# Kernel optimization log

Hardware: AMD Instinct MI355X
Metric: run time of the kernel (lower is better)

The kernel has to match this reference:

```python
import jax, jax.numpy as jnp
import numpy as np

D = 64      # in_features
U = 1024    # hidden units
B = 4096    # batch

def _build_masks():
    d0 = np.arange(D)
    dh = np.arange(U) % (D - 1)
    m0 = (d0[None, :] <= dh[:, None]).astype(np.float32)          # [U, D]
    m1 = (dh[None, :] <= dh[:, None]).astype(np.float32)          # [U, U]
    m2 = np.tile((dh[None, :] < d0[:, None]).astype(np.float32), (2, 1))  # [2D, U]
    return jnp.asarray(m0), jnp.asarray(m1), jnp.asarray(m2)


def setup_inputs() -> dict:
    key = jax.random.key(0)
    ks = jax.random.split(key, 7)
    scale = 0.02  # small init so exp(sigma) stays finite
    return {
        "u": jax.random.normal(ks[0], (B, D), dtype=jnp.float32),
        "W0": jax.random.normal(ks[1], (U, D), dtype=jnp.float32) * scale,
        "b0": jax.random.normal(ks[2], (U,), dtype=jnp.float32) * scale,
        "W1": jax.random.normal(ks[3], (U, U), dtype=jnp.float32) * scale,
        "b1": jax.random.normal(ks[4], (U,), dtype=jnp.float32) * scale,
        "W2": jax.random.normal(ks[5], (2 * D, U), dtype=jnp.float32) * scale,
        "b2": jax.random.normal(ks[6], (2 * D,), dtype=jnp.float32) * scale,
    }


def reference(u, W0, b0, W1, b1, W2, b2):
    m0, m1, m2 = _build_masks()
    mW0, mW1, mW2 = m0 * W0, m1 * W1, m2 * W2  # masked weights (constant across steps)

    def made(x):  # x: [B, D] -> mu, sigma each [B, D]
        h = jax.nn.relu(x @ mW0.T + b0)
        h = jax.nn.relu(h @ mW1.T + b1)
        z = h @ mW2.T + b2
        return z[:, :D], z[:, D:]

    def step(carry, i):
        x, ldj = carry
        mu, sigma = made(x)
        # ordering = arange(D) (sequential, not reversed) => idx == i
        x = x.at[:, i].set(u[:, i] * jnp.exp(sigma[:, i]) + mu[:, i])
        ldj = ldj.at[:, i].set(sigma[:, i])
        return (x, ldj), None

    x0 = jnp.zeros_like(u)
    ldj0 = jnp.zeros_like(u)
    (x, ldj), _ = jax.lax.scan(step, (x0, ldj0), jnp.arange(D))
    log_det_jacobian = jnp.sum(ldj, axis=1, keepdims=True)  # [B, 1]
    return x, log_det_jacobian
```

## Files before the change

### kernel.cpp

```cpp
#include <hip/hip_runtime.h>
#include <hip/hip_bf16.h>

#define BATCH 4096
#define NTHR 512

typedef __attribute__((ext_vector_type(8))) short bf16x8;
typedef __attribute__((ext_vector_type(4))) float f32x4;
typedef __attribute__((ext_vector_type(4))) short short4v;

#define BAR() asm volatile("s_waitcnt lgkmcnt(0)\n\ts_barrier" ::: "memory")

__host__ __device__ __forceinline__ int off1(int g) { return (g <= 16) ? 17 * g : 16 * g + 16; }
__host__ __device__ __forceinline__ int cntg(int g) { return (g < 16) ? 17 : 16; }
__host__ __device__ __forceinline__ int unitOf(int p) {
    int gp, jp;
    if (p < 272) { gp = p / 17; jp = p - gp * 17; }
    else         { gp = (p >> 4) - 1; jp = p & 15; }
    return gp + 63 * jp;
}
__device__ __forceinline__ short f2bf(float f) {
    __hip_bfloat16 h = __float2bfloat16(f);
    return *reinterpret_cast<short*>(&h);
}

__global__ void prep5(const float* __restrict__ W0, const float* __restrict__ b0,
                      const float* __restrict__ W1, const float* __restrict__ b1,
                      const float* __restrict__ W2,
                      short* __restrict__ W1f, short* __restrict__ W2f,
                      short* __restrict__ W0f, float* __restrict__ b1p) {
    __shared__ short ws[16][1024];
    const int b = blockIdx.x, t = threadIdx.x;
    if (b < 72) {
        const bool isW1 = (b < 64);
        const int n = t >> 4;
        int u;
        if (isW1) u = unitOf(b * 16 + n);
        else {
            const int c = b - 64;
            u = (n & 1) ? (64 + c * 8 + (n >> 1)) : (c * 8 + (n >> 1));
        }
        const float* src = isW1 ? (W1 + (long)u * 1024) : (W2 + (long)u * 1024);
        const int c0 = (t & 15) * 4;
#pragma unroll
        for (int j = 0; j < 16; ++j) {
            int c = c0 + j * 64;
            float4 v = *(const float4*)&src[c];
            short4v sv;
            sv[0] = f2bf(v.x); sv[1] = f2bf(v.y); sv[2] = f2bf(v.z); sv[3] = f2bf(v.w);
            *(short4v*)&ws[n][c] = sv;
        }
        __syncthreads();
#pragma unroll 1
        for (int it = 0; it < 16; ++it) {
            int v = t + it * 256;
            if (v < 4032) {
                int g = v >> 6, lane2 = v & 63;
                int nn = lane2 & 15, aq2 = lane2 >> 4;
                bf16x8 pk;
#pragma unroll
                for (int e = 0; e < 8; ++e) {
                    int k = aq2 * 8 + e;
                    pk[e] = (k < cntg(g)) ? ws[nn][g + 63 * k] : (short)0;
                }
                if (isW1) *(bf16x8*)&W1f[(((long)g * 64 + b) * 64 + lane2) * 8] = pk;
                else      *(bf16x8*)&W2f[(((long)g * 8 + (b - 64)) * 64 + lane2) * 8] = pk;
            }
        }
    } else if (b < 88) {
        const int bb = b - 72;
#pragma unroll 1
        for (int j = 0; j < 32; ++j) {
            int q = t + j * 256;
            if (q < 8064) {
                int idx = bb * 8064 + q;
                int g = idx >> 11, rem = idx & 2047;
                int n2 = rem >> 10, kt = (rem >> 9) & 1, lane2 = (rem >> 3) & 63, e = rem & 7;
                int sl = n2 * 16 + (lane2 & 15);
                int kp = kt * 32 + ((lane2 >> 4) << 3) + e;
                float val = 0.f;
                if (sl < cntg(g)) {
                    int u = unitOf(off1(g) + sl);
                    if (kp == 0) val = b0[u];
                    else if (kp - 1 <= g) val = W0[u * 64 + kp - 1];
                }
                W0f[idx] = f2bf(val);
            }
        }
    } else {
        for (int p = t; p < 1024; p += 256) b1p[p] = b1[unitOf(p)];
    }
}

__global__ __launch_bounds__(NTHR, 2) void made5(
    const float* __restrict__ uin, const float* __restrict__ b2,
    const short* __restrict__ W1f, const short* __restrict__ W2f,
    const short* __restrict__ W0f, const float* __restrict__ b1p,
    float* __restrict__ out) {

    __shared__ __align__(16) short h1g[16][40];
    __shared__ __align__(16) short h2g[16][40];
    __shared__ __align__(16) short xhist[16][80];
    __shared__ __align__(16) float uT[64][16];
    __shared__ __align__(16) float xLs[16][68];
    __shared__ float ldjpart[8][16];

    const int t = threadIdx.x, lane = t & 63, wv = t >> 6;
    const int n = lane & 15, aq = lane >> 4;
    const int rowbase = blockIdx.x * 16;

    {
        int* z1 = (int*)&h1g[0][0];
        for (int idx = t; idx < 16 * 40 / 2; idx += NTHR) z1[idx] = 0;
        int* z2 = (int*)&h2g[0][0];
        for (int idx = t; idx < 16 * 40 / 2; idx += NTHR) z2[idx] = 0;
        int* z3 = (int*)&xhist[0][0];
        for (int idx = t; idx < 16 * 80 / 2; idx += NTHR) z3[idx] = 0;
    }
    if (t < 256) {
        int r = t >> 4, c0 = (t & 15) * 4;
        float4 v = *(const float4*)&uin[(long)(rowbase + r) * 64 + c0];
        uT[c0 + 0][r] = v.x; uT[c0 + 1][r] = v.y; uT[c0 + 2][r] = v.z; uT[c0 + 3][r] = v.w;
    }

    f32x4 acc2[8];
#pragma unroll
    for (int s = 0; s < 8; ++s) {
        float bb = b1p[(wv * 8 + s) * 16 + n];
        acc2[s] = (f32x4){bb, bb, bb, bb};
    }
    f32x4 zacc;
    {
        int pc = wv * 16 + n;
        float bz = b2[(pc >> 1) + 64 * (pc & 1)];
        zacc = (f32x4){bz, bz, bz, bz};
    }

    bf16x8 w1fE[8], w1fO[8], w2fE, w2fO, w0f[4];
#pragma unroll
    for (int s = 0; s < 8; ++s) {
        w1fO[s] = *(const bf16x8*)&W1f[(((long)0 * 64 + (wv * 8 + s)) * 64 + lane) * 8];
        w1fE[s] = *(const bf16x8*)&W1f[(((long)1 * 64 + (wv * 8 + s)) * 64 + lane) * 8];
    }
    w2fO = *(const bf16x8*)&W2f[(((long)0 * 8 + wv) * 64 + lane) * 8];
    w2fE = *(const bf16x8*)&W2f[(((long)1 * 8 + wv) * 64 + lane) * 8];
    if (wv == 7) {
#pragma unroll
        for (int f = 0; f < 4; ++f)
            w0f[f] = *(const bf16x8*)&W0f[(((long)0 * 4 + f) * 64 + lane) * 8];
    }

    f32x4 ldjacc = {0.f, 0.f, 0.f, 0.f};
    float ureg[4];

    BAR();
    if (t < 16) xhist[t][0] = (short)0x3F80;
#pragma unroll
    for (int r = 0; r < 4; ++r)
        ureg[r] = uT[8 * wv + (n >> 1)][aq * 4 + r];

    auto body = [&](int i, bf16x8* w1fS, bf16x8& w2fS) {
        const int g = i - 1;

        if (g >= 0 && wv == 7) {
            const int cgg = cntg(g);
            const bool two_k = (g >= 31);
            const bf16x8 ax0 = *(const bf16x8*)&xhist[n][aq * 8];
            f32x4 d0 = {0.f, 0.f, 0.f, 0.f};
            d0 = __builtin_amdgcn_mfma_f32_16x16x32_bf16(ax0, w0f[0], d0, 0, 0, 0);
            f32x4 d1 = {0.f, 0.f, 0.f, 0.f};
            if (two_k) {
                const bf16x8 ax1 = *(const bf16x8*)&xhist[n][32 + aq * 8];
                d0 = __builtin_amdgcn_mfma_f32_16x16x32_bf16(ax1, w0f[1], d0, 0, 0, 0);
                if (cgg == 17) {
                    d1 = __builtin_amdgcn_mfma_f32_16x16x32_bf16(ax0, w0f[2], d1, 0, 0, 0);
                    d1 = __builtin_amdgcn_mfma_f32_16x16x32_bf16(ax1, w0f[3], d1, 0, 0, 0);
                }
            } else if (cgg == 17) {
                d1 = __builtin_amdgcn_mfma_f32_16x16x32_bf16(ax0, w0f[2], d1, 0, 0, 0);
            }
            {
                const int gW = (i < 63) ? i : 62;
#pragma unroll
                for (int f = 0; f < 4; ++f)
                    w0f[f] = *(const bf16x8*)&W0f[(((long)gW * 4 + f) * 64 + lane) * 8];
            }
#pragma unroll
            for (int r = 0; r < 4; ++r) {
                float v = d0[r];
                h1g[aq * 4 + r][n] = f2bf(v > 0.f ? v : 0.f);
            }
            if (n == 0) {
#pragma unroll
                for (int r = 0; r < 4; ++r) {
                    float v = (cgg == 17) ? (d1[r] > 0.f ? d1[r] : 0.f) : 0.f;
                    h1g[aq * 4 + r][16] = f2bf(v);
                }
            }
        }
        BAR();

        if (g >= 0) {
            const int og = off1(g), cg = cntg(g);
            const int tf0 = og >> 4, tfl = (og + cg - 1) >> 4;
            const bf16x8 af = *(const bf16x8*)&h1g[n][aq * 8];
            const int s0 = tf0 - wv * 8;
#pragma unroll
            for (int s = 0; s < 8; ++s) {
                if (s >= s0)
                    acc2[s] = __builtin_amdgcn_mfma_f32_16x16x32_bf16(af, w1fS[s], acc2[s], 0, 0, 0);
            }
            if (i >= 1) {
                const int gp = (i + 1 < 63) ? (i + 1) : 62;
                const int s0p = (off1(gp) >> 4) - wv * 8;
#pragma unroll
                for (int s = 0; s < 8; ++s) {
                    if (s >= s0p)
                        w1fS[s] = *(const bf16x8*)&W1f[(((long)gp * 64 + (wv * 8 + s)) * 64 + lane) * 8];
                }
            }
            if (wv == (tf0 >> 3)) {
                const int s = tf0 & 7;
                const int j = tf0 * 16 + n - og;
                if (j >= 0 && j < cg) {
#pragma unroll
                    for (int r = 0; r < 4; ++r) {
                        float v = acc2[s][r];
                        h2g[aq * 4 + r][j] = f2bf(v > 0.f ? v : 0.f);
                    }
                }
            }
            if (tfl != tf0 && wv == (tfl >> 3)) {
                const int s = tfl & 7;
                const int j = tfl * 16 + n - og;
                if (j < cg) {
#pragma unroll
                    for (int r = 0; r < 4; ++r) {
                        float v = acc2[s][r];
                        h2g[aq * 4 + r][j] = f2bf(v > 0.f ? v : 0.f);
                    }
                }
            }
            if (g == 16 && wv == 0 && n == 0) {
#pragma unroll
                for (int r = 0; r < 4; ++r) h2g[aq * 4 + r][16] = 0;
            }
        }
        BAR();

        if (g >= 0) {
            const bf16x8 af3 = *(const bf16x8*)&h2g[n][aq * 8];
            zacc = __builtin_amdgcn_mfma_f32_16x16x32_bf16(af3, w2fS, zacc, 0, 0, 0);
            if (i >= 1) {
                const int gp = (i + 1 < 63) ? (i + 1) : 62;
                w2fS = *(const bf16x8*)&W2f[(((long)gp * 8 + wv) * 64 + lane) * 8];
            }
        }
        if (wv == (i >> 3)) {
            const int n0 = 2 * (i & 7);
            f32x4 sgv;
#pragma unroll
            for (int r = 0; r < 4; ++r) sgv[r] = __shfl_xor(zacc[r], 1);
            if (n == n0) {
#pragma unroll
                for (int r = 0; r < 4; ++r) {
                    const float sg = sgv[r], mu = zacc[r];
                    const float x = ureg[r] * __expf(sg) + mu;
                    ldjacc[r] += sg;
                    const int m = aq * 4 + r;
                    xLs[m][i] = x;
                    if (i < 63) xhist[m][i + 1] = f2bf(x);
                }
            }
        }
        BAR();
    };

#pragma unroll 1
    for (int i = 0; i < 64; i += 2) {
        body(i, w1fE, w2fE);
        body(i + 1, w1fO, w2fO);
    }

#pragma unroll
    for (int r = 0; r < 4; ++r) {
        float v = ldjacc[r];
        v += __shfl_xor(v, 2);
        v += __shfl_xor(v, 4);
        v += __shfl_xor(v, 8);
        if (n == 0) ldjpart[wv][aq * 4 + r] = v;
    }
    BAR();

    if (t < 256) {
        int r = t >> 4, c = (t & 15) * 4;
        float4 v;
        v.x = xLs[r][c]; v.y = xLs[r][c + 1]; v.z = xLs[r][c + 2]; v.w = xLs[r][c + 3];
        *(float4*)&out[(long)(rowbase + r) * 64 + c] = v;
    }
    if (t < 16) {
        float s = 0.f;
#pragma unroll
        for (int w = 0; w < 8; ++w) s += ldjpart[w][t];
        out[(long)BATCH * 64 + rowbase + t] = s;
    }
}

extern "C" void kernel_launch(void* const* d_in, const int* in_sizes, int n_in,
                              void* d_out, int out_size, void* d_ws, size_t ws_size,
                              hipStream_t stream) {
    (void)in_sizes; (void)n_in; (void)out_size; (void)ws_size;
    const float* u  = (const float*)d_in[0];
    const float* W0 = (const float*)d_in[1];
    const float* b0 = (const float*)d_in[2];
    const float* W1 = (const float*)d_in[3];
    const float* b1 = (const float*)d_in[4];
    const float* W2 = (const float*)d_in[5];
    const float* b2 = (const float*)d_in[6];
    float* out = (float*)d_out;

    short* W1f = (short*)d_ws;
    short* W2f = (short*)((char*)d_ws + 4128768);
    short* W0f = (short*)((char*)d_ws + 4128768 + 516096);
    float* b1p = (float*)((char*)d_ws + 4128768 + 516096 + 258048);

    prep5<<<dim3(89), dim3(256), 0, stream>>>(W0, b0, W1, b1, W2, W1f, W2f, W0f, b1p);
    made5<<<dim3(BATCH / 16), dim3(NTHR), 0, stream>>>(u, b2, W1f, W2f, W0f, b1p, out);
}
```

Baseline: 209.5 us.

## Fuse layer-0 MFMA into x-update phase, interleave W1 tiles across waves

The layer-0 MFMA and its h1 write move out of their own barrier-separated phase and into the wave that just produced the new x column, which removes one barrier per step. W1 tile ownership changes from contiguous (wv*8+s) to strided (wv+8*s), so the growing active tile range is spread across all waves instead of landing on a few. The prep kernel is relaunched with 512 threads. The new schedule depends on wave wv==i>>3 seeing its own xhist write, and only one wave does the layer-0 work on the critical path.

```diff
diff --git a/kernel.cpp b/kernel.cpp
--- a/kernel.cpp
+++ b/kernel.cpp
@@ -23,7 +23,7 @@
     return *reinterpret_cast<short*>(&h);
 }
 
-__global__ void prep5(const float* __restrict__ W0, const float* __restrict__ b0,
+__global__ void prep6(const float* __restrict__ W0, const float* __restrict__ b0,
                       const float* __restrict__ W1, const float* __restrict__ b1,
                       const float* __restrict__ W2,
                       short* __restrict__ W1f, short* __restrict__ W2f,
@@ -32,18 +32,15 @@
     const int b = blockIdx.x, t = threadIdx.x;
     if (b < 72) {
         const bool isW1 = (b < 64);
-        const int n = t >> 4;
+        const int n = t >> 5;
         int u;
         if (isW1) u = unitOf(b * 16 + n);
-        else {
-            const int c = b - 64;
-            u = (n & 1) ? (64 + c * 8 + (n >> 1)) : (c * 8 + (n >> 1));
-        }
+        else { const int c = b - 64; u = (n & 1) ? (64 + c * 8 + (n >> 1)) : (c * 8 + (n >> 1)); }
         const float* src = isW1 ? (W1 + (long)u * 1024) : (W2 + (long)u * 1024);
-        const int c0 = (t & 15) * 4;
-#pragma unroll
-        for (int j = 0; j < 16; ++j) {
-            int c = c0 + j * 64;
+        const int c0 = (t & 31) * 4;
+#pragma unroll
+        for (int j = 0; j < 8; ++j) {
+            int c = c0 + j * 128;
             float4 v = *(const float4*)&src[c];
             short4v sv;
             sv[0] = f2bf(v.x); sv[1] = f2bf(v.y); sv[2] = f2bf(v.z); sv[3] = f2bf(v.w);
@@ -51,8 +48,8 @@
         }
         __syncthreads();
 #pragma unroll 1
-        for (int it = 0; it < 16; ++it) {
-            int v = t + it * 256;
+        for (int it = 0; it < 8; ++it) {
+            int v = t + it * 512;
             if (v < 4032) {
                 int g = v >> 6, lane2 = v & 63;
                 int nn = lane2 & 15, aq2 = lane2 >> 4;
@@ -69,8 +66,8 @@
     } else if (b < 88) {
         const int bb = b - 72;
 #pragma unroll 1
-        for (int j = 0; j < 32; ++j) {
-            int q = t + j * 256;
+        for (int j = 0; j < 16; ++j) {
+            int q = t + j * 512;
             if (q < 8064) {
                 int idx = bb * 8064 + q;
                 int g = idx >> 11, rem = idx & 2047;
@@ -87,11 +84,11 @@
             }
         }
     } else {
-        for (int p = t; p < 1024; p += 256) b1p[p] = b1[unitOf(p)];
-    }
-}
-
-__global__ __launch_bounds__(NTHR, 2) void made5(
+        for (int p = t; p < 1024; p += 512) b1p[p] = b1[unitOf(p)];
+    }
+}
+
+__global__ __launch_bounds__(NTHR, 2) void made6(
     const float* __restrict__ uin, const float* __restrict__ b2,
     const short* __restrict__ W1f, const short* __restrict__ W2f,
     const short* __restrict__ W0f, const float* __restrict__ b1p,
@@ -125,7 +122,7 @@
     f32x4 acc2[8];
 #pragma unroll
     for (int s = 0; s < 8; ++s) {
-        float bb = b1p[(wv * 8 + s) * 16 + n];
+        float bb = b1p[(wv + 8 * s) * 16 + n];
         acc2[s] = (f32x4){bb, bb, bb, bb};
     }
     f32x4 zacc;
@@ -135,107 +132,69 @@
         zacc = (f32x4){bz, bz, bz, bz};
     }
 
-    bf16x8 w1fE[8], w1fO[8], w2fE, w2fO, w0f[4];
+    bf16x8 w1fE[8], w1fO[8], w2fE, w2fO, w0f0, w0f1, w0f2;
 #pragma unroll
     for (int s = 0; s < 8; ++s) {
-        w1fO[s] = *(const bf16x8*)&W1f[(((long)0 * 64 + (wv * 8 + s)) * 64 + lane) * 8];
-        w1fE[s] = *(const bf16x8*)&W1f[(((long)1 * 64 + (wv * 8 + s)) * 64 + lane) * 8];
+        const int tile = wv + 8 * s;
+        w1fO[s] = *(const bf16x8*)&W1f[(((long)0 * 64 + tile) * 64 + lane) * 8];
+        w1fE[s] = *(const bf16x8*)&W1f[(((long)1 * 64 + tile) * 64 + lane) * 8];
     }
     w2fO = *(const bf16x8*)&W2f[(((long)0 * 8 + wv) * 64 + lane) * 8];
     w2fE = *(const bf16x8*)&W2f[(((long)1 * 8 + wv) * 64 + lane) * 8];
-    if (wv == 7) {
-#pragma unroll
-        for (int f = 0; f < 4; ++f)
-            w0f[f] = *(const bf16x8*)&W0f[(((long)0 * 4 + f) * 64 + lane) * 8];
+    {
+        const long gb = 8 * wv;
+        w0f0 = *(const bf16x8*)&W0f[((gb * 4 + 0) * 64 + lane) * 8];
+        w0f1 = *(const bf16x8*)&W0f[((gb * 4 + 1) * 64 + lane) * 8];
+        w0f2 = *(const bf16x8*)&W0f[((gb * 4 + 2) * 64 + lane) * 8];
     }
 
     f32x4 ldjacc = {0.f, 0.f, 0.f, 0.f};
-    float ureg[4];
-
     BAR();
     if (t < 16) xhist[t][0] = (short)0x3F80;
-#pragma unroll
-    for (int r = 0; r < 4; ++r)
-        ureg[r] = uT[8 * wv + (n >> 1)][aq * 4 + r];
+    float ureg[4];
+#pragma unroll
+    for (int r = 0; r < 4; ++r) ureg[r] = uT[8 * wv + (n >> 1)][aq * 4 + r];
 
     auto body = [&](int i, bf16x8* w1fS, bf16x8& w2fS) {
         const int g = i - 1;
-
-        if (g >= 0 && wv == 7) {
-            const int cgg = cntg(g);
-            const bool two_k = (g >= 31);
-            const bf16x8 ax0 = *(const bf16x8*)&xhist[n][aq * 8];
-            f32x4 d0 = {0.f, 0.f, 0.f, 0.f};
-            d0 = __builtin_amdgcn_mfma_f32_16x16x32_bf16(ax0, w0f[0], d0, 0, 0, 0);
-            f32x4 d1 = {0.f, 0.f, 0.f, 0.f};
-            if (two_k) {
-                const bf16x8 ax1 = *(const bf16x8*)&xhist[n][32 + aq * 8];
-                d0 = __builtin_amdgcn_mfma_f32_16x16x32_bf16(ax1, w0f[1], d0, 0, 0, 0);
-                if (cgg == 17) {
-                    d1 = __builtin_amdgcn_mfma_f32_16x16x32_bf16(ax0, w0f[2], d1, 0, 0, 0);
-                    d1 = __builtin_amdgcn_mfma_f32_16x16x32_bf16(ax1, w0f[3], d1, 0, 0, 0);
-                }
-            } else if (cgg == 17) {
-                d1 = __builtin_amdgcn_mfma_f32_16x16x32_bf16(ax0, w0f[2], d1, 0, 0, 0);
-            }
-            {
-                const int gW = (i < 63) ? i : 62;
-#pragma unroll
-                for (int f = 0; f < 4; ++f)
-                    w0f[f] = *(const bf16x8*)&W0f[(((long)gW * 4 + f) * 64 + lane) * 8];
-            }
-#pragma unroll
-            for (int r = 0; r < 4; ++r) {
-                float v = d0[r];
-                h1g[aq * 4 + r][n] = f2bf(v > 0.f ? v : 0.f);
-            }
-            if (n == 0) {
-#pragma unroll
-                for (int r = 0; r < 4; ++r) {
-                    float v = (cgg == 17) ? (d1[r] > 0.f ? d1[r] : 0.f) : 0.f;
-                    h1g[aq * 4 + r][16] = f2bf(v);
-                }
-            }
-        }
-        BAR();
-
         if (g >= 0) {
             const int og = off1(g), cg = cntg(g);
             const int tf0 = og >> 4, tfl = (og + cg - 1) >> 4;
-            const bf16x8 af = *(const bf16x8*)&h1g[n][aq * 8];
-            const int s0 = tf0 - wv * 8;
-#pragma unroll
-            for (int s = 0; s < 8; ++s) {
-                if (s >= s0)
-                    acc2[s] = __builtin_amdgcn_mfma_f32_16x16x32_bf16(af, w1fS[s], acc2[s], 0, 0, 0);
-            }
-            if (i >= 1) {
+            const int s0 = (tf0 > wv) ? ((tf0 - wv + 7) >> 3) : 0;
+            if (s0 < 8) {
+                const bf16x8 af = *(const bf16x8*)&h1g[n][aq * 8];
+#pragma unroll
+                for (int s = 0; s < 8; ++s)
+                    if (s >= s0)
+                        acc2[s] = __builtin_amdgcn_mfma_f32_16x16x32_bf16(af, w1fS[s], acc2[s], 0, 0, 0);
+            }
+            {
                 const int gp = (i + 1 < 63) ? (i + 1) : 62;
-                const int s0p = (off1(gp) >> 4) - wv * 8;
-#pragma unroll
-                for (int s = 0; s < 8; ++s) {
+                const int tf0p = off1(gp) >> 4;
+                const int s0p = (tf0p > wv) ? ((tf0p - wv + 7) >> 3) : 0;
+#pragma unroll
+                for (int s = 0; s < 8; ++s)
                     if (s >= s0p)
-                        w1fS[s] = *(const bf16x8*)&W1f[(((long)gp * 64 + (wv * 8 + s)) * 64 + lane) * 8];
-                }
-            }
-            if (wv == (tf0 >> 3)) {
-                const int s = tf0 & 7;
+                        w1fS[s] = *(const bf16x8*)&W1f[(((long)gp * 64 + (wv + 8 * s)) * 64 + lane) * 8];
+            }
+            if (wv == (tf0 & 7)) {
+                const int sT = tf0 >> 3;
                 const int j = tf0 * 16 + n - og;
                 if (j >= 0 && j < cg) {
 #pragma unroll
                     for (int r = 0; r < 4; ++r) {
-                        float v = acc2[s][r];
+                        float v = acc2[sT][r];
                         h2g[aq * 4 + r][j] = f2bf(v > 0.f ? v : 0.f);
                     }
                 }
             }
-            if (tfl != tf0 && wv == (tfl >> 3)) {
-                const int s = tfl & 7;
+            if (tfl != tf0 && wv == (tfl & 7)) {
+                const int sT = tfl >> 3;
                 const int j = tfl * 16 + n - og;
                 if (j < cg) {
 #pragma unroll
                     for (int r = 0; r < 4; ++r) {
-                        float v = acc2[s][r];
+                        float v = acc2[sT][r];
                         h2g[aq * 4 + r][j] = f2bf(v > 0.f ? v : 0.f);
                     }
                 }
@@ -246,14 +205,11 @@
             }
         }
         BAR();
-
         if (g >= 0) {
             const bf16x8 af3 = *(const bf16x8*)&h2g[n][aq * 8];
             zacc = __builtin_amdgcn_mfma_f32_16x16x32_bf16(af3, w2fS, zacc, 0, 0, 0);
-            if (i >= 1) {
-                const int gp = (i + 1 < 63) ? (i + 1) : 62;
-                w2fS = *(const bf16x8*)&W2f[(((long)gp * 8 + wv) * 64 + lane) * 8];
-            }
+            const int gp = (i + 1 < 63) ? (i + 1) : 62;
+            w2fS = *(const bf16x8*)&W2f[(((long)gp * 8 + wv) * 64 + lane) * 8];
         }
         if (wv == (i >> 3)) {
             const int n0 = 2 * (i & 7);
@@ -269,6 +225,36 @@
                     const int m = aq * 4 + r;
                     xLs[m][i] = x;
                     if (i < 63) xhist[m][i + 1] = f2bf(x);
+                }
+            }
+            if (i < 63) {
+                const bf16x8 ax0 = *(const bf16x8*)&xhist[n][aq * 8];
+                f32x4 d0 = {0.f, 0.f, 0.f, 0.f};
+                d0 = __builtin_amdgcn_mfma_f32_16x16x32_bf16(ax0, w0f0, d0, 0, 0, 0);
+                if (i >= 31) {
+                    const bf16x8 ax1 = *(const bf16x8*)&xhist[n][32 + aq * 8];
+                    d0 = __builtin_amdgcn_mfma_f32_16x16x32_bf16(ax1, w0f1, d0, 0, 0, 0);
+                }
+                f32x4 d1 = {0.f, 0.f, 0.f, 0.f};
+                if (i < 16)
+                    d1 = __builtin_amdgcn_mfma_f32_16x16x32_bf16(ax0, w0f2, d1, 0, 0, 0);
+#pragma unroll
+                for (int r = 0; r < 4; ++r) {
+                    float v = d0[r];
+                    h1g[aq * 4 + r][n] = f2bf(v > 0.f ? v : 0.f);
+                }
+                if (n == 0) {
+#pragma unroll
+                    for (int r = 0; r < 4; ++r) {
+                        float v = (i < 16) ? (d1[r] > 0.f ? d1[r] : 0.f) : 0.f;
+                        h1g[aq * 4 + r][16] = f2bf(v);
+                    }
+                }
+                if (i + 1 < 63 && ((i + 1) >> 3) == wv) {
+                    const long gb = i + 1;
+                    w0f0 = *(const bf16x8*)&W0f[((gb * 4 + 0) * 64 + lane) * 8];
+                    w0f1 = *(const bf16x8*)&W0f[((gb * 4 + 1) * 64 + lane) * 8];
+                    w0f2 = *(const bf16x8*)&W0f[((gb * 4 + 2) * 64 + lane) * 8];
                 }
             }
         }
@@ -323,6 +309,6 @@
     short* W0f = (short*)((char*)d_ws + 4128768 + 516096);
     float* b1p = (float*)((char*)d_ws + 4128768 + 516096 + 258048);
 
-    prep5<<<dim3(89), dim3(256), 0, stream>>>(W0, b0, W1, b1, W2, W1f, W2f, W0f, b1p);
-    made5<<<dim3(BATCH / 16), dim3(NTHR), 0, stream>>>(u, b2, W1f, W2f, W0f, b1p, out);
-}
+    prep6<<<dim3(89), dim3(512), 0, stream>>>(W0, b0, W1, b1, W2, W1f, W2f, W0f, b1p);
+    made6<<<dim3(BATCH / 16), dim3(NTHR), 0, stream>>>(u, b2, W1f, W2f, W0f, b1p, out);
+}
```

Result: faster. 176.4 us (-15.8%).
